# Kernel optimization log

Measured on AMD Instinct MI355X. Metric: run time of the kernel, lower is better.

The kernel has to match this reference:

```python
import jax, jax.numpy as jnp
import numpy as np


def _pair_table(L):
    # 0,0 0,1 ... upper-triangular (start,end) enumeration, P = L*(L+1)/2
    starts = np.concatenate([np.arange(i + 1) for i in range(L)])
    ends = np.concatenate([np.full(i + 1, i) for i in range(L)])
    return starts.astype(np.int32), ends.astype(np.int32)


def setup_inputs() -> dict:
    key = jax.random.key(0)
    ks = jax.random.split(key, 10)
    B, L, Q, H, T = 8, 384, 64, 256, 9
    p = lambda k, shape: jax.random.normal(k, shape, jnp.float32) * 0.02
    return dict(
        batch_hiddens=jax.random.normal(ks[0], (B, L, H), jnp.float32),
        batch_masks=jnp.ones((B, L), dtype=bool),
        queries=jax.random.normal(ks[1], (B, Q, H), jnp.float32),
        queries_locs=jax.random.uniform(ks[2], (B, Q, 2), jnp.float32) * L,
        queries_logits=jax.random.normal(ks[3], (B, Q, T + 1), jnp.float32),
        Wc=p(ks[4], (H, T + 1)), bc=jnp.zeros((T + 1,), jnp.float32),
        Wq=p(ks[5], (H, 2 * H)), bq=jnp.zeros((2 * H,), jnp.float32),
        Wv=p(ks[6], (H, 2 * H)), bv=jnp.zeros((2 * H,), jnp.float32),
        Wo=p(ks[7], (H, 2)), bo=jnp.zeros((2,), jnp.float32),
        Wf=p(ks[8], (H, 2)), bf=jnp.zeros((2,), jnp.float32),
    )


def reference(batch_hiddens, batch_masks, queries, queries_locs, queries_logits,
              Wc, bc, Wq, bq, Wv, bv, Wo, bo, Wf, bf):
    B, L, H = batch_hiddens.shape
    Q = queries.shape[1]
    starts, ends = _pair_table(L)  # static: L known at trace time

    # label probabilities: softmax(prior logits + classifier(queries))
    labels_pros = jax.nn.softmax(queries_logits + queries @ Wc + bc, axis=-1)

    # biaffine start/end channels
    qh = (queries @ Wq + bq).reshape(B, Q, 2, H)        # [B,Q,2,H]
    ch = (batch_hiddens @ Wv + bv).reshape(B, L, 2, H)  # [B,L,2,H]
    score = jnp.einsum('bqch,bvch->bcqv', qh, ch) / jnp.sqrt(jnp.float32(H))
    score = jnp.where(batch_masks[:, None, None, :], score, -1e8)

    # span score via start/end table gather: [B,Q,P]
    span = score[:, 0][:, :, starts] + score[:, 1][:, :, ends]
    mask_p = batch_masks[:, ends]  # [B,P] valid if end token valid

    # locator: gaussian distribution over spans centered at refined locations
    offset = queries @ Wo + bo                      # [B,Q,2]
    factors = jax.nn.softplus(queries @ Wf + bf)    # [B,Q,2] positive widths
    locs = queries_locs + offset                    # [B,Q,2]
    pairs_f = jnp.stack([jnp.asarray(starts), jnp.asarray(ends)], axis=-1).astype(jnp.float32)  # [P,2]
    d2 = (pairs_f[None, None] - locs[:, :, None]) ** 2          # [B,Q,P,2]
    weight = jnp.exp(-(d2 * factors[:, :, None]).sum(-1))       # [B,Q,P]
    weight = jnp.where(mask_p[:, None, :], weight, 0.0)

    # weighted softmax over spans
    m = jnp.max(span, axis=-1, keepdims=True)
    e = jnp.exp(span - m) * weight
    locs_pros = e / (jnp.sum(e, axis=-1, keepdims=True) + 1e-12)
    return labels_pros, locs_pros
```

## Files before the change

kernel.cpp:

```cpp
#include <hip/hip_runtime.h>
#include <math.h>

#define B_    8
#define L_    384
#define Q_    64
#define H_    256
#define R_    512
#define P_    73920
#define NF4   18480
#define QF4   4620

#define WS_EXEY  0
#define WS_W2    0
#define WS_D     131072
#define WS_WB    131584
#define WS_E2    132096
#define WS_TAB   393216
#define WS_HIDT  411904
#define WS_G     1198336
#define WS_DOTC  1460480
#define WS_LOCS  1461504
#define WS_FACT  1462528

__global__ __launch_bounds__(512) void k_setup(const float* __restrict__ hid,
                                               const float* __restrict__ Wq,
                                               const float* __restrict__ bq,
                                               const float* __restrict__ Wv,
                                               const float* __restrict__ bv,
                                               float* __restrict__ ws) {
    __shared__ float smem[64 * 65];
    int blk = blockIdx.x, tid = threadIdx.x;

    if (blk < 64) {
        int h0 = blk * 4;
        int c = tid >> 8, hv = tid & 255;
        int cu = __builtin_amdgcn_readfirstlane(c);
        const float4* wv4  = reinterpret_cast<const float4*>(Wv + hv * 512 + cu * 256);
        const float4* wq40 = reinterpret_cast<const float4*>(Wq + (h0 + 0) * 512 + cu * 256);
        const float4* wq41 = reinterpret_cast<const float4*>(Wq + (h0 + 1) * 512 + cu * 256);
        const float4* wq42 = reinterpret_cast<const float4*>(Wq + (h0 + 2) * 512 + cu * 256);
        const float4* wq43 = reinterpret_cast<const float4*>(Wq + (h0 + 3) * 512 + cu * 256);
        float a0 = 0.f, a1 = 0.f, a2 = 0.f, a3 = 0.f;
        for (int k = 0; k < 64; k++) {
            float4 wv = wv4[k];
            float4 w0 = wq40[k]; a0 += wv.x * w0.x + wv.y * w0.y + wv.z * w0.z + wv.w * w0.w;
            float4 w1 = wq41[k]; a1 += wv.x * w1.x + wv.y * w1.y + wv.z * w1.z + wv.w * w1.w;
            float4 w2 = wq42[k]; a2 += wv.x * w2.x + wv.y * w2.y + wv.z * w2.z + wv.w * w2.w;
            float4 w3 = wq43[k]; a3 += wv.x * w3.x + wv.y * w3.y + wv.z * w3.z + wv.w * w3.w;
        }
        ws[WS_W2 + (h0 + 0) * 512 + tid] = a0;
        ws[WS_W2 + (h0 + 1) * 512 + tid] = a1;
        ws[WS_W2 + (h0 + 2) * 512 + tid] = a2;
        ws[WS_W2 + (h0 + 3) * 512 + tid] = a3;
        if (tid < 128) {
            int c2 = tid >> 6, lane = tid & 63;
#pragma unroll
            for (int hh = 0; hh < 4; hh++) {
                float v = 0.f;
#pragma unroll
                for (int k2 = 0; k2 < 4; k2++) {
                    int hp = lane + 64 * k2;
                    v += Wq[(h0 + hh) * 512 + c2 * 256 + hp] * bv[c2 * 256 + hp];
                }
#pragma unroll
                for (int off = 32; off; off >>= 1) v += __shfl_xor(v, off);
                if (lane == 0) ws[WS_WB + c2 * 256 + h0 + hh] = v;
            }
        }
    } else if (blk < 101) {
        int idx = (blk - 64) * 512 + tid;
        if (idx < NF4) {
            int p0 = idx << 2;
            int e = (int)((sqrtf(8.f * (float)p0 + 1.f) - 1.f) * 0.5f);
            int tri = (e * (e + 1)) >> 1;
            while (tri > p0) { e--; tri -= (e + 1); }
            while (p0 - tri > e) { tri += (e + 1); e++; }
            int s = p0 - tri;
            reinterpret_cast<unsigned*>(ws)[WS_TAB + idx] = ((unsigned)e << 16) | (unsigned)s;
        }
    } else if (blk == 101) {
        int c = tid >> 8, hv = tid & 255;
        int cu = __builtin_amdgcn_readfirstlane(c);
        const float4* wv4 = reinterpret_cast<const float4*>(Wv + hv * 512 + cu * 256);
        const float4* bq4 = reinterpret_cast<const float4*>(bq + cu * 256);
        float a = 0.f;
        for (int k = 0; k < 64; k++) {
            float4 wv = wv4[k]; float4 b4 = bq4[k];
            a += wv.x * b4.x + wv.y * b4.y + wv.z * b4.z + wv.w * b4.w;
        }
        ws[WS_D + tid] = a;
        if (tid < 128) {
            int c2 = tid >> 6, lane = tid & 63;
            float v = 0.f;
#pragma unroll
            for (int k2 = 0; k2 < 4; k2++) {
                int hp = lane + 64 * k2;
                v += bq[c2 * 256 + hp] * bv[c2 * 256 + hp];
            }
#pragma unroll
            for (int off = 32; off; off >>= 1) v += __shfl_xor(v, off);
            if (lane == 0) ws[WS_E2 + c2] = v;
        }
    } else {
        int t = blk - 102;
        int b = t / 24, tt = t % 24;
        int mt = tt % 6, nt = tt / 6;
        const float* in = hid + b * 98304;
        float* outp = ws + WS_HIDT + b * 98304;
        float (*tsm)[65] = (float(*)[65])smem;
        int lane = tid & 63, row8 = tid >> 6;
        int m0 = mt * 64, n0 = nt * 64;
#pragma unroll
        for (int p = 0; p < 8; p++) {
            int mr = p * 8 + row8;
            tsm[mr][lane] = in[(m0 + mr) * 256 + n0 + lane];
        }
        __syncthreads();
#pragma unroll
        for (int p = 0; p < 8; p++) {
            int nr = p * 8 + row8;
            outp[(n0 + nr) * 384 + m0 + lane] = tsm[lane][nr];
        }
    }
}

__global__ __launch_bounds__(512) void k_g(const float* __restrict__ queries,
                                           const float* __restrict__ qlocs,
                                           const float* __restrict__ qlogits,
                                           const float* __restrict__ Wc,
                                           const float* __restrict__ bc,
                                           const float* __restrict__ Wo,
                                           const float* __restrict__ bo,
                                           const float* __restrict__ Wf,
                                           const float* __restrict__ bf,
                                           float* __restrict__ ws,
                                           float* __restrict__ out) {
    int tid = threadIdx.x;
    int r0 = blockIdx.x * 2;

    {
        const float* qa = queries + r0 * 256;
        const float* qb = qa + 256;
        const float* w2 = ws + WS_W2 + tid;
        float a0 = 0.f, a1 = 0.f;
#pragma unroll 8
        for (int h = 0; h < 256; h++) {
            float w = w2[h * 512];
            a0 += qa[h] * w;
            a1 += qb[h] * w;
        }
        float dj = ws[WS_D + tid];
        ws[WS_G + r0 * 512 + tid]       = a0 + dj;
        ws[WS_G + (r0 + 1) * 512 + tid] = a1 + dj;
    }

    int w = tid >> 6, lane = tid & 63;
    if (w < 4) {
        int r = r0 + (w >> 1), c = w & 1;
        float v = 0.f;
#pragma unroll
        for (int k = 0; k < 4; k++) {
            int h = lane + 64 * k;
            v += queries[r * 256 + h] * ws[WS_WB + c * 256 + h];
        }
#pragma unroll
        for (int off = 32; off; off >>= 1) v += __shfl_xor(v, off);
        if (lane == 0) ws[WS_DOTC + r * 2 + c] = v + ws[WS_E2 + c];
    } else if (w < 6) {
        int r = r0 + (w - 4);
        const float* qr = queries + r * 256;
        float q0 = qr[lane], q1 = qr[lane + 64], q2 = qr[lane + 128], q3 = qr[lane + 192];

        float x[10];
#pragma unroll
        for (int t = 0; t < 10; t++) {
            float v = q0 * Wc[lane * 10 + t] + q1 * Wc[(lane + 64) * 10 + t]
                    + q2 * Wc[(lane + 128) * 10 + t] + q3 * Wc[(lane + 192) * 10 + t];
#pragma unroll
            for (int off = 32; off; off >>= 1) v += __shfl_xor(v, off);
            x[t] = qlogits[r * 10 + t] + bc[t] + v;
        }
        float m = -1e30f;
#pragma unroll
        for (int t = 0; t < 10; t++) m = fmaxf(m, x[t]);
        float s = 0.f;
#pragma unroll
        for (int t = 0; t < 10; t++) { x[t] = expf(x[t] - m); s += x[t]; }
        float inv = 1.0f / s;
        if (lane == 0) {
#pragma unroll
            for (int t = 0; t < 10; t++) out[r * 10 + t] = x[t] * inv;
        }

#pragma unroll
        for (int k = 0; k < 2; k++) {
            float vo = q0 * Wo[lane * 2 + k] + q1 * Wo[(lane + 64) * 2 + k]
                     + q2 * Wo[(lane + 128) * 2 + k] + q3 * Wo[(lane + 192) * 2 + k];
            float vf = q0 * Wf[lane * 2 + k] + q1 * Wf[(lane + 64) * 2 + k]
                     + q2 * Wf[(lane + 128) * 2 + k] + q3 * Wf[(lane + 192) * 2 + k];
#pragma unroll
            for (int off = 32; off; off >>= 1) { vo += __shfl_xor(vo, off); vf += __shfl_xor(vf, off); }
            if (lane == 0) {
                ws[WS_LOCS + r * 2 + k] = qlocs[r * 2 + k] + vo + bo[k];
                float xx = vf + bf[k];
                ws[WS_FACT + r * 2 + k] = (xx > 20.f) ? xx : log1pf(expf(xx));
            }
        }
    }
}

__global__ __launch_bounds__(384) void k_prep(const float* __restrict__ ws_c,
                                              float* __restrict__ ws,
                                              const int* __restrict__ mask) {
    __shared__ float s0[384], s1[384];
    __shared__ float Ex[384], Ey[384];
    __shared__ float scal[4];

    int tid = threadIdx.x;
    int r = blockIdx.x;
    int b = r >> 6;

    const float* gp = ws_c + WS_G + r * 512;
    float dotc0 = ws_c[WS_DOTC + r * 2 + 0];
    float dotc1 = ws_c[WS_DOTC + r * 2 + 1];
    float lx = ws_c[WS_LOCS + r * 2 + 0], ly = ws_c[WS_LOCS + r * 2 + 1];
    float fx = ws_c[WS_FACT + r * 2 + 0], fy = ws_c[WS_FACT + r * 2 + 1];

    const float* hT = ws_c + WS_HIDT + b * 98304;
    float s0r, s1r;
    bool mk;
    {
        int v = tid;
        float a0 = 0.f, a1 = 0.f;
        const float* p = hT + v;
#pragma unroll 8
        for (int h = 0; h < 256; h++) {
            float x = p[h * 384];
            a0 += x * gp[h];
            a1 += x * gp[256 + h];
        }
        mk = mask[b * 384 + v] != 0;
        s0r = mk ? (a0 + dotc0) * 0.0625f : -1e8f;
        s1r = mk ? (a1 + dotc1) * 0.0625f : -1e8f;
        s0[v] = s0r;
        s1[v] = s1r;
    }
    __syncthreads();

    if (tid < 64) {
        int l = tid;
        float p[6];
        p[0] = s0[l * 6 + 0];
#pragma unroll
        for (int k = 1; k < 6; k++) p[k] = fmaxf(p[k - 1], s0[l * 6 + k]);
        float run = p[5];
#pragma unroll
        for (int off = 1; off < 64; off <<= 1) {
            float t = __shfl_up(run, off);
            if (l >= off) run = fmaxf(run, t);
        }
        float excl = __shfl_up(run, 1);
        if (l == 0) excl = -1e30f;
        float m0 = __shfl(run, 63);
        float lm = -1e30f, lm1 = -1e30f;
#pragma unroll
        for (int k = 0; k < 6; k++) {
            float pm = fmaxf(excl, p[k]);
            float sv = s1[l * 6 + k];
            lm = fmaxf(lm, sv + pm);
            lm1 = fmaxf(lm1, sv);
        }
#pragma unroll
        for (int off = 1; off < 64; off <<= 1) {
            lm  = fmaxf(lm,  __shfl_xor(lm,  off));
            lm1 = fmaxf(lm1, __shfl_xor(lm1, off));
        }
        if (l == 0) { scal[0] = m0; scal[1] = lm1; scal[2] = lm; }
    }
    __syncthreads();

    float m0 = scal[0], m1 = scal[1], mM = scal[2];
    float exv, eyv;
    {
        int i = tid;
        float ds = (float)i - lx;
        exv = expf(s0r - m0 - fx * ds * ds);
        float de = (float)i - ly;
        eyv = mk ? expf(s1r - m1 - fy * de * de) : 0.f;
        Ex[i] = exv;
        Ey[i] = eyv;
    }
    __syncthreads();

    if (tid < 64) {
        int l = tid;
        float p[6];
        p[0] = Ex[l * 6 + 0];
#pragma unroll
        for (int k = 1; k < 6; k++) p[k] = p[k - 1] + Ex[l * 6 + k];
        float run = p[5];
#pragma unroll
        for (int off = 1; off < 64; off <<= 1) {
            float t = __shfl_up(run, off);
            if (l >= off) run += t;
        }
        float excl = __shfl_up(run, 1);
        if (l == 0) excl = 0.f;
        float s2l = 0.f;
#pragma unroll
        for (int k = 0; k < 6; k++)
            s2l += Ey[l * 6 + k] * (excl + p[k]);
#pragma unroll
        for (int off = 1; off < 64; off <<= 1) s2l += __shfl_xor(s2l, off);
        if (l == 0) {
            float C = expf(m0 + m1 - mM);
            scal[3] = C / (C * s2l + 1e-12f);
        }
    }
    __syncthreads();

    float scale = scal[3];
    float* exr = ws + WS_EXEY + r * 768;
    exr[tid]       = exv;
    exr[384 + tid] = eyv * scale;
}

__global__ __launch_bounds__(256) void k_write(const float* __restrict__ ws,
                                               float* __restrict__ out) {
    __shared__ alignas(16) float exsh[4][384];
    __shared__ float eysh[384];
    int tid = threadIdx.x;
    int r = blockIdx.x >> 2, q = blockIdx.x & 3;
    const float* exr = ws + WS_EXEY + r * 768;
    for (int i = tid; i < 768; i += 256) {
        float v = exr[i];
        if (i < 384) {
#pragma unroll
            for (int c = 0; c < 4; c++)
                if (i >= c) exsh[c][i - c] = v;
        } else {
            eysh[i - 384] = v;
        }
    }
    __syncthreads();

    const unsigned* tab = reinterpret_cast<const unsigned*>(ws) + WS_TAB;
    float* ob = out + 5120 + r * 73920;
    int base = q * QF4;
    int end = base + QF4;
    for (int idx = base + tid; idx < end; idx += 256) {
        unsigned t = tab[idx];
        int e = (int)(t >> 16), s = (int)(t & 0xffffu);
        float4 v;
        if (s + 3 <= e) {
            float ey = eysh[e];
            const float4* p4 = reinterpret_cast<const float4*>(&exsh[s & 3][s & ~3]);
            float4 ex = *p4;
            v.x = ex.x * ey; v.y = ex.y * ey; v.z = ex.z * ey; v.w = ex.w * ey;
        } else {
            int ss = s, ee = e;
            float ey = eysh[ee];
            v.x = exsh[0][ss] * ey; if (++ss > ee) { ss = 0; ey = eysh[++ee]; }
            v.y = exsh[0][ss] * ey; if (++ss > ee) { ss = 0; ey = eysh[++ee]; }
            v.z = exsh[0][ss] * ey; if (++ss > ee) { ss = 0; ey = eysh[++ee]; }
            v.w = exsh[0][ss] * ey;
        }
        reinterpret_cast<float4*>(ob)[idx] = v;
    }
}

extern "C" void kernel_launch(void* const* d_in, const int* in_sizes, int n_in,
                              void* d_out, int out_size, void* d_ws, size_t ws_size,
                              hipStream_t stream) {
    const float* hiddens = (const float*)d_in[0];
    const int* masks     = (const int*)d_in[1];
    const float* queries = (const float*)d_in[2];
    const float* qlocs   = (const float*)d_in[3];
    const float* qlogits = (const float*)d_in[4];
    const float* Wc = (const float*)d_in[5];
    const float* bc = (const float*)d_in[6];
    const float* Wq = (const float*)d_in[7];
    const float* bq = (const float*)d_in[8];
    const float* Wv = (const float*)d_in[9];
    const float* bv = (const float*)d_in[10];
    const float* Wo = (const float*)d_in[11];
    const float* bo = (const float*)d_in[12];
    const float* Wf = (const float*)d_in[13];
    const float* bf = (const float*)d_in[14];
    float* out = (float*)d_out;
    float* ws  = (float*)d_ws;

    hipLaunchKernelGGL(k_setup, dim3(294),  dim3(512), 0, stream, hiddens, Wq, bq, Wv, bv, ws);
    hipLaunchKernelGGL(k_g,     dim3(256),  dim3(512), 0, stream,
                       queries, qlocs, qlogits, Wc, bc, Wo, bo, Wf, bf, ws, out);
    hipLaunchKernelGGL(k_prep,  dim3(512),  dim3(384), 0, stream, ws, ws, masks);
    hipLaunchKernelGGL(k_write, dim3(2048), dim3(256), 0, stream, ws, out);
}
```

Baseline: 239.6 us.

## Fuse query projection, span prep and output write into one per-row kernel

Merges k_g, k_prep and k_write into a single kernel with one 384-thread block per (batch, query) row. The projected query vector, scalar terms and the ex/ey vectors now stay in shared memory instead of passing through global workspace, which removes two launches and the intermediate global round-trips. In exchange, the large output write is spread over 512 blocks instead of 2048, which lowers parallelism for the bandwidth-bound store phase. The G projection also loses its two-rows-per-block reuse of the W2 loads.

```diff
diff --git a/kernel.cpp b/kernel.cpp
--- a/kernel.cpp
+++ b/kernel.cpp
@@ -8,19 +8,13 @@
 #define R_    512
 #define P_    73920
 #define NF4   18480
-#define QF4   4620
-
-#define WS_EXEY  0
+
 #define WS_W2    0
 #define WS_D     131072
 #define WS_WB    131584
 #define WS_E2    132096
 #define WS_TAB   393216
 #define WS_HIDT  411904
-#define WS_G     1198336
-#define WS_DOTC  1460480
-#define WS_LOCS  1461504
-#define WS_FACT  1462528
 
 __global__ __launch_bounds__(512) void k_setup(const float* __restrict__ hid,
                                                const float* __restrict__ Wq,
@@ -124,74 +118,53 @@
     }
 }
 
-__global__ __launch_bounds__(512) void k_g(const float* __restrict__ queries,
-                                           const float* __restrict__ qlocs,
-                                           const float* __restrict__ qlogits,
-                                           const float* __restrict__ Wc,
-                                           const float* __restrict__ bc,
-                                           const float* __restrict__ Wo,
-                                           const float* __restrict__ bo,
-                                           const float* __restrict__ Wf,
-                                           const float* __restrict__ bf,
-                                           float* __restrict__ ws,
-                                           float* __restrict__ out) {
+__global__ __launch_bounds__(384) void k_fused(const float* __restrict__ queries,
+                                               const float* __restrict__ qlocs,
+                                               const float* __restrict__ qlogits,
+                                               const float* __restrict__ Wc,
+                                               const float* __restrict__ bc,
+                                               const float* __restrict__ Wo,
+                                               const float* __restrict__ bo,
+                                               const float* __restrict__ Wf,
+                                               const float* __restrict__ bf,
+                                               const int* __restrict__ mask,
+                                               const float* __restrict__ ws,
+                                               float* __restrict__ out) {
+    __shared__ float g0[256], g1[256];
+    __shared__ float s0[384], s1[384];
+    __shared__ float Exs[384], Eys[384];
+    __shared__ alignas(16) float exsh[4][384];
+    __shared__ float eysh[384];
+    __shared__ float sc2[12];
+
     int tid = threadIdx.x;
-    int r0 = blockIdx.x * 2;
-
-    {
-        const float* qa = queries + r0 * 256;
-        const float* qb = qa + 256;
-        const float* w2 = ws + WS_W2 + tid;
-        float a0 = 0.f, a1 = 0.f;
+    int r = blockIdx.x;
+    int b = r >> 6;
+    const float* qr = queries + r * 256;
+
+    for (int j = tid; j < 512; j += 384) {
+        const float* w2 = ws + WS_W2 + j;
+        float a = 0.f;
 #pragma unroll 8
-        for (int h = 0; h < 256; h++) {
-            float w = w2[h * 512];
-            a0 += qa[h] * w;
-            a1 += qb[h] * w;
-        }
-        float dj = ws[WS_D + tid];
-        ws[WS_G + r0 * 512 + tid]       = a0 + dj;
-        ws[WS_G + (r0 + 1) * 512 + tid] = a1 + dj;
+        for (int h = 0; h < 256; h++) a += qr[h] * w2[h * 512];
+        a += ws[WS_D + j];
+        if (j < 256) g0[j] = a; else g1[j - 256] = a;
     }
 
     int w = tid >> 6, lane = tid & 63;
-    if (w < 4) {
-        int r = r0 + (w >> 1), c = w & 1;
+    if (w < 2) {
+        int c = w;
         float v = 0.f;
 #pragma unroll
         for (int k = 0; k < 4; k++) {
             int h = lane + 64 * k;
-            v += queries[r * 256 + h] * ws[WS_WB + c * 256 + h];
+            v += qr[h] * ws[WS_WB + c * 256 + h];
         }
 #pragma unroll
         for (int off = 32; off; off >>= 1) v += __shfl_xor(v, off);
-        if (lane == 0) ws[WS_DOTC + r * 2 + c] = v + ws[WS_E2 + c];
-    } else if (w < 6) {
-        int r = r0 + (w - 4);
-        const float* qr = queries + r * 256;
+        if (lane == 0) sc2[c] = v + ws[WS_E2 + c];
+    } else if (w == 2) {
         float q0 = qr[lane], q1 = qr[lane + 64], q2 = qr[lane + 128], q3 = qr[lane + 192];
-
-        float x[10];
-#pragma unroll
-        for (int t = 0; t < 10; t++) {
-            float v = q0 * Wc[lane * 10 + t] + q1 * Wc[(lane + 64) * 10 + t]
-                    + q2 * Wc[(lane + 128) * 10 + t] + q3 * Wc[(lane + 192) * 10 + t];
-#pragma unroll
-            for (int off = 32; off; off >>= 1) v += __shfl_xor(v, off);
-            x[t] = qlogits[r * 10 + t] + bc[t] + v;
-        }
-        float m = -1e30f;
-#pragma unroll
-        for (int t = 0; t < 10; t++) m = fmaxf(m, x[t]);
-        float s = 0.f;
-#pragma unroll
-        for (int t = 0; t < 10; t++) { x[t] = expf(x[t] - m); s += x[t]; }
-        float inv = 1.0f / s;
-        if (lane == 0) {
-#pragma unroll
-            for (int t = 0; t < 10; t++) out[r * 10 + t] = x[t] * inv;
-        }
-
 #pragma unroll
         for (int k = 0; k < 2; k++) {
             float vo = q0 * Wo[lane * 2 + k] + q1 * Wo[(lane + 64) * 2 + k]
@@ -201,49 +174,56 @@
 #pragma unroll
             for (int off = 32; off; off >>= 1) { vo += __shfl_xor(vo, off); vf += __shfl_xor(vf, off); }
             if (lane == 0) {
-                ws[WS_LOCS + r * 2 + k] = qlocs[r * 2 + k] + vo + bo[k];
+                sc2[2 + k] = qlocs[r * 2 + k] + vo + bo[k];
                 float xx = vf + bf[k];
-                ws[WS_FACT + r * 2 + k] = (xx > 20.f) ? xx : log1pf(expf(xx));
+                sc2[4 + k] = (xx > 20.f) ? xx : log1pf(expf(xx));
             }
         }
-    }
-}
-
-__global__ __launch_bounds__(384) void k_prep(const float* __restrict__ ws_c,
-                                              float* __restrict__ ws,
-                                              const int* __restrict__ mask) {
-    __shared__ float s0[384], s1[384];
-    __shared__ float Ex[384], Ey[384];
-    __shared__ float scal[4];
-
-    int tid = threadIdx.x;
-    int r = blockIdx.x;
-    int b = r >> 6;
-
-    const float* gp = ws_c + WS_G + r * 512;
-    float dotc0 = ws_c[WS_DOTC + r * 2 + 0];
-    float dotc1 = ws_c[WS_DOTC + r * 2 + 1];
-    float lx = ws_c[WS_LOCS + r * 2 + 0], ly = ws_c[WS_LOCS + r * 2 + 1];
-    float fx = ws_c[WS_FACT + r * 2 + 0], fy = ws_c[WS_FACT + r * 2 + 1];
-
-    const float* hT = ws_c + WS_HIDT + b * 98304;
+    } else if (w == 3) {
+        float q0 = qr[lane], q1 = qr[lane + 64], q2 = qr[lane + 128], q3 = qr[lane + 192];
+        float x[10];
+#pragma unroll
+        for (int t = 0; t < 10; t++) {
+            float v = q0 * Wc[lane * 10 + t] + q1 * Wc[(lane + 64) * 10 + t]
+                    + q2 * Wc[(lane + 128) * 10 + t] + q3 * Wc[(lane + 192) * 10 + t];
+#pragma unroll
+            for (int off = 32; off; off >>= 1) v += __shfl_xor(v, off);
+            x[t] = qlogits[r * 10 + t] + bc[t] + v;
+        }
+        float m = -1e30f;
+#pragma unroll
+        for (int t = 0; t < 10; t++) m = fmaxf(m, x[t]);
+        float s = 0.f;
+#pragma unroll
+        for (int t = 0; t < 10; t++) { x[t] = expf(x[t] - m); s += x[t]; }
+        float inv = 1.0f / s;
+        if (lane == 0) {
+#pragma unroll
+            for (int t = 0; t < 10; t++) out[r * 10 + t] = x[t] * inv;
+        }
+    }
+    __syncthreads();
+
+    float dotc0 = sc2[0], dotc1 = sc2[1];
+    float lx = sc2[2], ly = sc2[3], fx = sc2[4], fy = sc2[5];
+
+    const float* hT = ws + WS_HIDT + b * 98304;
     float s0r, s1r;
     bool mk;
     {
-        int v = tid;
         float a0 = 0.f, a1 = 0.f;
-        const float* p = hT + v;
+        const float* p = hT + tid;
 #pragma unroll 8
         for (int h = 0; h < 256; h++) {
             float x = p[h * 384];
-            a0 += x * gp[h];
-            a1 += x * gp[256 + h];
-        }
-        mk = mask[b * 384 + v] != 0;
+            a0 += x * g0[h];
+            a1 += x * g1[h];
+        }
+        mk = mask[b * 384 + tid] != 0;
         s0r = mk ? (a0 + dotc0) * 0.0625f : -1e8f;
         s1r = mk ? (a1 + dotc1) * 0.0625f : -1e8f;
-        s0[v] = s0r;
-        s1[v] = s1r;
+        s0[tid] = s0r;
+        s1[tid] = s1r;
     }
     __syncthreads();
 
@@ -275,29 +255,28 @@
             lm  = fmaxf(lm,  __shfl_xor(lm,  off));
             lm1 = fmaxf(lm1, __shfl_xor(lm1, off));
         }
-        if (l == 0) { scal[0] = m0; scal[1] = lm1; scal[2] = lm; }
-    }
-    __syncthreads();
-
-    float m0 = scal[0], m1 = scal[1], mM = scal[2];
+        if (l == 0) { sc2[6] = m0; sc2[7] = lm1; sc2[8] = lm; }
+    }
+    __syncthreads();
+
+    float m0 = sc2[6], m1 = sc2[7], mM = sc2[8];
     float exv, eyv;
     {
-        int i = tid;
-        float ds = (float)i - lx;
+        float ds = (float)tid - lx;
         exv = expf(s0r - m0 - fx * ds * ds);
-        float de = (float)i - ly;
+        float de = (float)tid - ly;
         eyv = mk ? expf(s1r - m1 - fy * de * de) : 0.f;
-        Ex[i] = exv;
-        Ey[i] = eyv;
+        Exs[tid] = exv;
+        Eys[tid] = eyv;
     }
     __syncthreads();
 
     if (tid < 64) {
         int l = tid;
         float p[6];
-        p[0] = Ex[l * 6 + 0];
-#pragma unroll
-        for (int k = 1; k < 6; k++) p[k] = p[k - 1] + Ex[l * 6 + k];
+        p[0] = Exs[l * 6 + 0];
+#pragma unroll
+        for (int k = 1; k < 6; k++) p[k] = p[k - 1] + Exs[l * 6 + k];
         float run = p[5];
 #pragma unroll
         for (int off = 1; off < 64; off <<= 1) {
@@ -309,46 +288,28 @@
         float s2l = 0.f;
 #pragma unroll
         for (int k = 0; k < 6; k++)
-            s2l += Ey[l * 6 + k] * (excl + p[k]);
+            s2l += Eys[l * 6 + k] * (excl + p[k]);
 #pragma unroll
         for (int off = 1; off < 64; off <<= 1) s2l += __shfl_xor(s2l, off);
         if (l == 0) {
             float C = expf(m0 + m1 - mM);
-            scal[3] = C / (C * s2l + 1e-12f);
-        }
-    }
-    __syncthreads();
-
-    float scale = scal[3];
-    float* exr = ws + WS_EXEY + r * 768;
-    exr[tid]       = exv;
-    exr[384 + tid] = eyv * scale;
-}
-
-__global__ __launch_bounds__(256) void k_write(const float* __restrict__ ws,
-                                               float* __restrict__ out) {
-    __shared__ alignas(16) float exsh[4][384];
-    __shared__ float eysh[384];
-    int tid = threadIdx.x;
-    int r = blockIdx.x >> 2, q = blockIdx.x & 3;
-    const float* exr = ws + WS_EXEY + r * 768;
-    for (int i = tid; i < 768; i += 256) {
-        float v = exr[i];
-        if (i < 384) {
-#pragma unroll
-            for (int c = 0; c < 4; c++)
-                if (i >= c) exsh[c][i - c] = v;
-        } else {
-            eysh[i - 384] = v;
-        }
+            sc2[9] = C / (C * s2l + 1e-12f);
+        }
+    }
+    __syncthreads();
+
+    {
+        float scale = sc2[9];
+#pragma unroll
+        for (int c = 0; c < 4; c++)
+            if (tid >= c) exsh[c][tid - c] = exv;
+        eysh[tid] = eyv * scale;
     }
     __syncthreads();
 
     const unsigned* tab = reinterpret_cast<const unsigned*>(ws) + WS_TAB;
     float* ob = out + 5120 + r * 73920;
-    int base = q * QF4;
-    int end = base + QF4;
-    for (int idx = base + tid; idx < end; idx += 256) {
+    for (int idx = tid; idx < NF4; idx += 384) {
         unsigned t = tab[idx];
         int e = (int)(t >> 16), s = (int)(t & 0xffffu);
         float4 v;
@@ -390,9 +351,7 @@
     float* out = (float*)d_out;
     float* ws  = (float*)d_ws;
 
-    hipLaunchKernelGGL(k_setup, dim3(294),  dim3(512), 0, stream, hiddens, Wq, bq, Wv, bv, ws);
-    hipLaunchKernelGGL(k_g,     dim3(256),  dim3(512), 0, stream,
-                       queries, qlocs, qlogits, Wc, bc, Wo, bo, Wf, bf, ws, out);
-    hipLaunchKernelGGL(k_prep,  dim3(512),  dim3(384), 0, stream, ws, ws, masks);
-    hipLaunchKernelGGL(k_write, dim3(2048), dim3(256), 0, stream, ws, out);
+    hipLaunchKernelGGL(k_setup, dim3(294), dim3(512), 0, stream, hiddens, Wq, bq, Wv, bv, ws);
+    hipLaunchKernelGGL(k_fused, dim3(512), dim3(384), 0, stream,
+                       queries, qlocs, qlogits, Wc, bc, Wo, bo, Wf, bf, masks, ws, out);
 }
```

After: 240.4 us. Within noise of the previous version (+0.3%).
